# Performance work log

Measured on AMD Instinct MI355X. Metric: run time of the kernel, lower is better.

Reference implementation:

```python
import jax, jax.numpy as jnp
import numpy as np

B, T, T_OUT, D = 32, 2048, 512, 256
LN_EPS = 1e-5


def _ragged_adaptive_avg_pool(mu_mel, mel_lengths, target_lens):
    """Vectorized per-sample adaptive_avg_pool1d over ragged lengths.

    For sample b with input length L=mel_lengths[b] and output length
    O=target_lens[b], output bin j averages input frames
    [floor(j*L/O), ceil((j+1)*L/O)). Bins j >= O are zero (pad_sequence).
    Returns [B, T_OUT, D].
    """
    j = jnp.arange(T_OUT, dtype=jnp.int32)[None, :, None]   # [1, T_OUT, 1]
    t = jnp.arange(T, dtype=jnp.int32)[None, None, :]       # [1, 1, T]
    L = mel_lengths.astype(jnp.int32)[:, None, None]        # [B, 1, 1]
    O = target_lens.astype(jnp.int32)[:, None, None]        # [B, 1, 1]
    start = (j * L) // O                                     # [B, T_OUT, 1]
    end = ((j + 1) * L + O - 1) // O                         # ceil division
    valid = j < O
    w = ((t >= start) & (t < end) & valid).astype(mu_mel.dtype)  # [B, T_OUT, T]
    cnt = jnp.maximum(end - start, 1).astype(mu_mel.dtype)
    w = w / cnt
    return jnp.einsum('bjt,btd->bjd', w, mu_mel)             # [B, T_OUT, D]


def setup_inputs() -> dict:
    key = jax.random.key(0)
    k1, k2, k3, k4 = jax.random.split(key, 4)
    mu_mel = jax.random.normal(k1, (B, T, D), dtype=jnp.float32)
    mel_lengths = jax.random.randint(k2, (B,), T // 2, T + 1, dtype=jnp.int32)
    target_lens = jax.random.randint(k3, (B,), T_OUT // 2, T_OUT + 1, dtype=jnp.int32)
    conv_w = jax.random.normal(k4, (D, D), dtype=jnp.float32) * (1.0 / np.sqrt(D))
    gamma = jnp.ones((D,), dtype=jnp.float32)
    beta = jnp.zeros((D,), dtype=jnp.float32)
    return {"mu_mel": mu_mel, "mel_lengths": mel_lengths,
            "target_lens": target_lens, "conv_w": conv_w,
            "gamma": gamma, "beta": beta}


def reference(mu_mel, mel_lengths, target_lens, conv_w, gamma, beta):
    # ragged adaptive avg pool + pad into [B, T_OUT, D]; torch wraps this in
    # no_grad, so stop_gradient mirrors that.
    pooled = jax.lax.stop_gradient(
        _ragged_adaptive_avg_pool(mu_mel, mel_lengths, target_lens))
    # 1x1 Conv1d (no bias) == per-position matmul, then exact GELU
    h = jax.nn.gelu(jnp.einsum('bjd,ed->bje', pooled, conv_w), approximate=False)
    # LayerNorm over D (applied to padded positions too, as in torch)
    mean = jnp.mean(h, axis=-1, keepdims=True)
    var = jnp.mean(jnp.square(h - mean), axis=-1, keepdims=True)
    return (h - mean) * jax.lax.rsqrt(var + LN_EPS) * gamma + beta
```

## Files before the change

kernel.cpp:

```cpp
#include <hip/hip_runtime.h>

#define NB 32
#define NT 2048
#define TOUT 512
#define ND 256
#define TILE_M 16
#define BLK_J 64
#define LDA 264
#define LDH 264

typedef __attribute__((ext_vector_type(4))) float f32x4;
typedef __attribute__((ext_vector_type(8))) short bf16x8;
typedef __attribute__((ext_vector_type(4))) unsigned short u16x4;

__device__ __forceinline__ unsigned short f2b(float f) {
    unsigned int u = __builtin_bit_cast(unsigned int, f);
    return (unsigned short)((u + 0x7FFFu + ((u >> 16) & 1u)) >> 16);
}

__device__ __forceinline__ float gelu_exact(float x) {
    return 0.5f * x * (1.0f + erff(x * 0.70710678118654752440f));
}

template <int K>
__device__ __forceinline__ f32x4 sumK(const float* p) {
    f32x4 v[K];
    #pragma unroll
    for (int t = 0; t < K; ++t)
        v[t] = *reinterpret_cast<const f32x4*>(p + (size_t)t * ND);
    f32x4 s = v[0];
    #pragma unroll
    for (int t = 1; t < K; ++t) s += v[t];
    return s;
}

__global__ __launch_bounds__(256, 6)
void pool_kernel(const float* __restrict__ mu,
                 const int* __restrict__ lens,
                 const int* __restrict__ olens,
                 const float* __restrict__ wf,
                 unsigned short* __restrict__ wbF,
                 unsigned short* __restrict__ pooled)
{
    const int tid  = (int)threadIdx.x;
    const int lane = tid & 63;
    const int wv   = tid >> 6;

    if (blockIdx.y == TOUT / 4) {
        const int gid = blockIdx.x * 256 + tid;
        const int l   = gid & 63;
        const int kk  = (gid >> 6) & 7;
        const int et  = gid >> 9;
        const int e   = et * 16 + (l & 15);
        const int k   = kk * 32 + (l >> 4) * 8;
        f32x4 a = *reinterpret_cast<const f32x4*>(wf + e * ND + k);
        f32x4 c = *reinterpret_cast<const f32x4*>(wf + e * ND + k + 4);
        u16x4 p0, p1;
        p0.x = f2b(a.x); p0.y = f2b(a.y); p0.z = f2b(a.z); p0.w = f2b(a.w);
        p1.x = f2b(c.x); p1.y = f2b(c.y); p1.z = f2b(c.z); p1.w = f2b(c.w);
        *reinterpret_cast<u16x4*>(wbF + (size_t)gid * 8)     = p0;
        *reinterpret_cast<u16x4*>(wbF + (size_t)gid * 8 + 4) = p1;
        return;
    }

    const int b = blockIdx.x;
    const int j = blockIdx.y * 4 + wv;
    const int L = lens[b];
    const int O = olens[b];

    f32x4 s = {0.f, 0.f, 0.f, 0.f};
    if (j < O) {
        const int st  = (j * L) / O;
        const int en  = ((j + 1) * L + O - 1) / O;
        const int cnt = en - st;
        const float* p = mu + (size_t)(b * NT + st) * ND + lane * 4;
        switch (cnt) {
            case 2: s = sumK<2>(p); break;
            case 3: s = sumK<3>(p); break;
            case 4: s = sumK<4>(p); break;
            case 5: s = sumK<5>(p); break;
            case 6: s = sumK<6>(p); break;
            case 7: s = sumK<7>(p); break;
            case 8: s = sumK<8>(p); break;
            case 9: s = sumK<9>(p); break;
            default:
                for (int t = 0; t < cnt; ++t)
                    s += *reinterpret_cast<const f32x4*>(p + (size_t)t * ND);
                break;
        }
        s *= 1.0f / (float)cnt;
    }
    u16x4 q;
    q.x = f2b(s.x); q.y = f2b(s.y); q.z = f2b(s.z); q.w = f2b(s.w);
    *reinterpret_cast<u16x4*>(pooled + ((size_t)b * TOUT + j) * ND + lane * 4) = q;
}

__global__ __launch_bounds__(512, 2)
void mm_kernel(const unsigned short* __restrict__ pooled,
               const unsigned short* __restrict__ wbF,
               const float* __restrict__ gamma,
               const float* __restrict__ beta,
               float* __restrict__ out)
{
    __shared__ unsigned short a_lds[TILE_M * LDA];
    __shared__ float h_lds[TILE_M * LDH];

    const int b    = blockIdx.x;
    const int jb   = blockIdx.y * BLK_J;
    const int tid  = (int)threadIdx.x;
    const int lane = tid & 63;
    const int wv   = tid >> 6;
    const int r    = lane & 15;
    const int kg   = lane >> 4;

    bf16x8 wreg[8][2];
    #pragma unroll
    for (int kk = 0; kk < 8; ++kk)
        #pragma unroll
        for (int p = 0; p < 2; ++p) {
            const int et = wv * 2 + p;
            wreg[kk][p] = *reinterpret_cast<const bf16x8*>(
                wbF + (size_t)((et * 8 + kk) * 64 + lane) * 8);
        }

    const f32x4 g4 = *reinterpret_cast<const f32x4*>(&gamma[lane * 4]);
    const f32x4 b4 = *reinterpret_cast<const f32x4*>(&beta[lane * 4]);

    for (int jt = 0; jt < BLK_J / TILE_M; ++jt) {
        const int j0 = jb + jt * TILE_M;

        const unsigned short* prow = pooled + ((size_t)b * TOUT + j0) * ND;
        #pragma unroll
        for (int it = 0; it < 2; ++it) {
            const int u  = it * 512 + tid;
            const int m  = u >> 6;
            const int dd = (u & 63) * 4;
            *reinterpret_cast<u16x4*>(&a_lds[m * LDA + dd]) =
                *reinterpret_cast<const u16x4*>(prow + (size_t)u * 4);
        }
        __syncthreads();

        f32x4 acc[2];
        acc[0] = (f32x4){0.f, 0.f, 0.f, 0.f};
        acc[1] = (f32x4){0.f, 0.f, 0.f, 0.f};
        #pragma unroll
        for (int kk = 0; kk < 8; ++kk) {
            const int k0 = kk * 32 + kg * 8;
            bf16x8 af = *reinterpret_cast<const bf16x8*>(&a_lds[r * LDA + k0]);
            acc[0] = __builtin_amdgcn_mfma_f32_16x16x32_bf16(af, wreg[kk][0], acc[0], 0, 0, 0);
            acc[1] = __builtin_amdgcn_mfma_f32_16x16x32_bf16(af, wreg[kk][1], acc[1], 0, 0, 0);
        }

        #pragma unroll
        for (int p = 0; p < 2; ++p) {
            const int col = wv * 32 + p * 16 + r;
            #pragma unroll
            for (int q = 0; q < 4; ++q)
                h_lds[(kg * 4 + q) * LDH + col] = gelu_exact(acc[p][q]);
        }
        __syncthreads();

        #pragma unroll
        for (int i = 0; i < 2; ++i) {
            const int m = wv + i * 8;
            f32x4 v = *reinterpret_cast<const f32x4*>(&h_lds[m * LDH + lane * 4]);
            float s  = v.x + v.y + v.z + v.w;
            float sq = v.x * v.x + v.y * v.y + v.z * v.z + v.w * v.w;
            #pragma unroll
            for (int off = 32; off > 0; off >>= 1) {
                s  += __shfl_xor(s, off, 64);
                sq += __shfl_xor(sq, off, 64);
            }
            const float mean = s * (1.0f / 256.0f);
            const float var  = sq * (1.0f / 256.0f) - mean * mean;
            const float rs   = rsqrtf(var + 1e-5f);
            f32x4 o = (v - mean) * rs * g4 + b4;
            *reinterpret_cast<f32x4*>(&out[((size_t)(b * TOUT) + j0 + m) * ND + lane * 4]) = o;
        }
        __syncthreads();
    }
}

__global__ __launch_bounds__(256, 4)
void fused_fallback(const float* __restrict__ mu,
                    const int* __restrict__ lens,
                    const int* __restrict__ olens,
                    const float* __restrict__ wf,
                    const float* __restrict__ gamma,
                    const float* __restrict__ beta,
                    float* __restrict__ out)
{
    __shared__ unsigned short a_lds[TILE_M * LDA];
    __shared__ float h_lds[TILE_M * LDH];

    const int b    = blockIdx.x;
    const int j0   = blockIdx.y * TILE_M;
    const int tid  = (int)threadIdx.x;
    const int lane = tid & 63;
    const int wv   = tid >> 6;
    const int L = lens[b];
    const int O = olens[b];

    for (int m = wv; m < TILE_M; m += 4) {
        const int j = j0 + m;
        f32x4 acc = {0.f, 0.f, 0.f, 0.f};
        if (j < O) {
            const int s = (j * L) / O;
            const int e = ((j + 1) * L + O - 1) / O;
            const float* src = mu + (size_t)(b * NT + s) * ND + lane * 4;
            for (int t = s; t < e; ++t) {
                acc += *reinterpret_cast<const f32x4*>(src);
                src += ND;
            }
            acc *= (1.0f / (float)(e - s));
        }
        u16x4 p;
        p.x = f2b(acc.x); p.y = f2b(acc.y); p.z = f2b(acc.z); p.w = f2b(acc.w);
        *reinterpret_cast<u16x4*>(&a_lds[m * LDA + lane * 4]) = p;
    }
    __syncthreads();

    const int r  = lane & 15;
    const int kg = lane >> 4;
    const int e0 = wv * 64;
    f32x4 acc[4];
    #pragma unroll
    for (int c = 0; c < 4; ++c) acc[c] = (f32x4){0.f, 0.f, 0.f, 0.f};
    #pragma unroll
    for (int kk = 0; kk < 8; ++kk) {
        const int k0 = kk * 32 + kg * 8;
        bf16x8 af = *reinterpret_cast<const bf16x8*>(&a_lds[r * LDA + k0]);
        #pragma unroll
        for (int ct = 0; ct < 4; ++ct) {
            const int e = e0 + ct * 16 + r;
            f32x4 w0 = *reinterpret_cast<const f32x4*>(&wf[e * ND + k0]);
            f32x4 w1 = *reinterpret_cast<const f32x4*>(&wf[e * ND + k0 + 4]);
            union { bf16x8 v; unsigned short u[8]; } cv;
            cv.u[0] = f2b(w0.x); cv.u[1] = f2b(w0.y);
            cv.u[2] = f2b(w0.z); cv.u[3] = f2b(w0.w);
            cv.u[4] = f2b(w1.x); cv.u[5] = f2b(w1.y);
            cv.u[6] = f2b(w1.z); cv.u[7] = f2b(w1.w);
            acc[ct] = __builtin_amdgcn_mfma_f32_16x16x32_bf16(af, cv.v, acc[ct], 0, 0, 0);
        }
    }
    #pragma unroll
    for (int ct = 0; ct < 4; ++ct) {
        const int col  = e0 + ct * 16 + r;
        const int row0 = kg * 4;
        #pragma unroll
        for (int q = 0; q < 4; ++q)
            h_lds[(row0 + q) * LDH + col] = gelu_exact(acc[ct][q]);
    }
    __syncthreads();
    const f32x4 g4 = *reinterpret_cast<const f32x4*>(&gamma[lane * 4]);
    const f32x4 b4 = *reinterpret_cast<const f32x4*>(&beta[lane * 4]);
    #pragma unroll
    for (int i = 0; i < 4; ++i) {
        const int m = wv + i * 4;
        f32x4 v = *reinterpret_cast<const f32x4*>(&h_lds[m * LDH + lane * 4]);
        float s  = v.x + v.y + v.z + v.w;
        float sq = v.x * v.x + v.y * v.y + v.z * v.z + v.w * v.w;
        #pragma unroll
        for (int off = 32; off > 0; off >>= 1) {
            s  += __shfl_xor(s, off, 64);
            sq += __shfl_xor(sq, off, 64);
        }
        const float mean = s * (1.0f / 256.0f);
        const float var  = sq * (1.0f / 256.0f) - mean * mean;
        const float rs   = rsqrtf(var + 1e-5f);
        f32x4 o = (v - mean) * rs * g4 + b4;
        *reinterpret_cast<f32x4*>(&out[((size_t)(b * TOUT) + j0 + m) * ND + lane * 4]) = o;
    }
}

extern "C" void kernel_launch(void* const* d_in, const int* in_sizes, int n_in,
                              void* d_out, int out_size, void* d_ws, size_t ws_size,
                              hipStream_t stream) {
    const float* mu    = (const float*)d_in[0];
    const int*   lens  = (const int*)d_in[1];
    const int*   olens = (const int*)d_in[2];
    const float* wf    = (const float*)d_in[3];
    const float* gamma = (const float*)d_in[4];
    const float* beta  = (const float*)d_in[5];
    float* out = (float*)d_out;

    const size_t wb_elems = (size_t)ND * ND;
    const size_t pooled_elems = (size_t)NB * TOUT * ND;
    const size_t need = (wb_elems + pooled_elems) * sizeof(unsigned short);

    if (ws_size >= need) {
        unsigned short* wbF    = (unsigned short*)d_ws;
        unsigned short* pooled = wbF + wb_elems;
        pool_kernel<<<dim3(NB, TOUT / 4 + 1), dim3(256), 0, stream>>>(
            mu, lens, olens, wf, wbF, pooled);
        mm_kernel<<<dim3(NB, TOUT / BLK_J), dim3(512), 0, stream>>>(
            pooled, wbF, gamma, beta, out);
    } else {
        fused_fallback<<<dim3(NB, TOUT / TILE_M), dim3(256), 0, stream>>>(
            mu, lens, olens, wf, gamma, beta, out);
    }
}
```

Baseline: 28.95 us.

## Fuse ragged pooling into matmul kernel, split weight conversion into tiny kernel

After: 26.31 us. 9.1% less time.

```diff
diff --git a/kernel.cpp b/kernel.cpp
--- a/kernel.cpp
+++ b/kernel.cpp
@@ -5,7 +5,6 @@
 #define TOUT 512
 #define ND 256
 #define TILE_M 16
-#define BLK_J 64
 #define LDA 264
 #define LDH 264
 
@@ -34,79 +33,37 @@
     return s;
 }
 
-__global__ __launch_bounds__(256, 6)
-void pool_kernel(const float* __restrict__ mu,
-                 const int* __restrict__ lens,
-                 const int* __restrict__ olens,
-                 const float* __restrict__ wf,
-                 unsigned short* __restrict__ wbF,
-                 unsigned short* __restrict__ pooled)
-{
-    const int tid  = (int)threadIdx.x;
-    const int lane = tid & 63;
-    const int wv   = tid >> 6;
-
-    if (blockIdx.y == TOUT / 4) {
-        const int gid = blockIdx.x * 256 + tid;
-        const int l   = gid & 63;
-        const int kk  = (gid >> 6) & 7;
-        const int et  = gid >> 9;
-        const int e   = et * 16 + (l & 15);
-        const int k   = kk * 32 + (l >> 4) * 8;
-        f32x4 a = *reinterpret_cast<const f32x4*>(wf + e * ND + k);
-        f32x4 c = *reinterpret_cast<const f32x4*>(wf + e * ND + k + 4);
-        u16x4 p0, p1;
-        p0.x = f2b(a.x); p0.y = f2b(a.y); p0.z = f2b(a.z); p0.w = f2b(a.w);
-        p1.x = f2b(c.x); p1.y = f2b(c.y); p1.z = f2b(c.z); p1.w = f2b(c.w);
-        *reinterpret_cast<u16x4*>(wbF + (size_t)gid * 8)     = p0;
-        *reinterpret_cast<u16x4*>(wbF + (size_t)gid * 8 + 4) = p1;
-        return;
-    }
-
-    const int b = blockIdx.x;
-    const int j = blockIdx.y * 4 + wv;
-    const int L = lens[b];
-    const int O = olens[b];
-
-    f32x4 s = {0.f, 0.f, 0.f, 0.f};
-    if (j < O) {
-        const int st  = (j * L) / O;
-        const int en  = ((j + 1) * L + O - 1) / O;
-        const int cnt = en - st;
-        const float* p = mu + (size_t)(b * NT + st) * ND + lane * 4;
-        switch (cnt) {
-            case 2: s = sumK<2>(p); break;
-            case 3: s = sumK<3>(p); break;
-            case 4: s = sumK<4>(p); break;
-            case 5: s = sumK<5>(p); break;
-            case 6: s = sumK<6>(p); break;
-            case 7: s = sumK<7>(p); break;
-            case 8: s = sumK<8>(p); break;
-            case 9: s = sumK<9>(p); break;
-            default:
-                for (int t = 0; t < cnt; ++t)
-                    s += *reinterpret_cast<const f32x4*>(p + (size_t)t * ND);
-                break;
-        }
-        s *= 1.0f / (float)cnt;
-    }
-    u16x4 q;
-    q.x = f2b(s.x); q.y = f2b(s.y); q.z = f2b(s.z); q.w = f2b(s.w);
-    *reinterpret_cast<u16x4*>(pooled + ((size_t)b * TOUT + j) * ND + lane * 4) = q;
+__global__ __launch_bounds__(512)
+void cvt_w_kernel(const float* __restrict__ wf, unsigned short* __restrict__ wbF) {
+    const int gid = blockIdx.x * 512 + (int)threadIdx.x;
+    const int l   = gid & 63;
+    const int kk  = (gid >> 6) & 7;
+    const int et  = gid >> 9;
+    const int e   = et * 16 + (l & 15);
+    const int k   = kk * 32 + (l >> 4) * 8;
+    f32x4 a = *reinterpret_cast<const f32x4*>(wf + e * ND + k);
+    f32x4 c = *reinterpret_cast<const f32x4*>(wf + e * ND + k + 4);
+    u16x4 p0, p1;
+    p0.x = f2b(a.x); p0.y = f2b(a.y); p0.z = f2b(a.z); p0.w = f2b(a.w);
+    p1.x = f2b(c.x); p1.y = f2b(c.y); p1.z = f2b(c.z); p1.w = f2b(c.w);
+    *reinterpret_cast<u16x4*>(wbF + (size_t)gid * 8)     = p0;
+    *reinterpret_cast<u16x4*>(wbF + (size_t)gid * 8 + 4) = p1;
 }
 
 __global__ __launch_bounds__(512, 2)
-void mm_kernel(const unsigned short* __restrict__ pooled,
-               const unsigned short* __restrict__ wbF,
-               const float* __restrict__ gamma,
-               const float* __restrict__ beta,
-               float* __restrict__ out)
+void fused_kernel(const float* __restrict__ mu,
+                  const int* __restrict__ lens,
+                  const int* __restrict__ olens,
+                  const unsigned short* __restrict__ wbF,
+                  const float* __restrict__ gamma,
+                  const float* __restrict__ beta,
+                  float* __restrict__ out)
 {
     __shared__ unsigned short a_lds[TILE_M * LDA];
     __shared__ float h_lds[TILE_M * LDH];
 
     const int b    = blockIdx.x;
-    const int jb   = blockIdx.y * BLK_J;
+    const int j0   = blockIdx.y * TILE_M;
     const int tid  = (int)threadIdx.x;
     const int lane = tid & 63;
     const int wv   = tid >> 6;
@@ -123,61 +80,79 @@
                 wbF + (size_t)((et * 8 + kk) * 64 + lane) * 8);
         }
 
+    const int L = lens[b];
+    const int O = olens[b];
+
+    #pragma unroll
+    for (int i = 0; i < 2; ++i) {
+        const int m = wv + i * 8;
+        const int j = j0 + m;
+        f32x4 s = {0.f, 0.f, 0.f, 0.f};
+        if (j < O) {
+            const int st  = (j * L) / O;
+            const int en  = ((j + 1) * L + O - 1) / O;
+            const int cnt = en - st;
+            const float* p = mu + (size_t)(b * NT + st) * ND + lane * 4;
+            switch (cnt) {
+                case 2: s = sumK<2>(p); break;
+                case 3: s = sumK<3>(p); break;
+                case 4: s = sumK<4>(p); break;
+                case 5: s = sumK<5>(p); break;
+                case 6: s = sumK<6>(p); break;
+                case 7: s = sumK<7>(p); break;
+                case 8: s = sumK<8>(p); break;
+                case 9: s = sumK<9>(p); break;
+                default:
+                    for (int t = 0; t < cnt; ++t)
+                        s += *reinterpret_cast<const f32x4*>(p + (size_t)t * ND);
+                    break;
+            }
+            s *= 1.0f / (float)cnt;
+        }
+        u16x4 q;
+        q.x = f2b(s.x); q.y = f2b(s.y); q.z = f2b(s.z); q.w = f2b(s.w);
+        *reinterpret_cast<u16x4*>(&a_lds[m * LDA + lane * 4]) = q;
+    }
+    __syncthreads();
+
+    f32x4 acc[2];
+    acc[0] = (f32x4){0.f, 0.f, 0.f, 0.f};
+    acc[1] = (f32x4){0.f, 0.f, 0.f, 0.f};
+    #pragma unroll
+    for (int kk = 0; kk < 8; ++kk) {
+        const int k0 = kk * 32 + kg * 8;
+        bf16x8 af = *reinterpret_cast<const bf16x8*>(&a_lds[r * LDA + k0]);
+        acc[0] = __builtin_amdgcn_mfma_f32_16x16x32_bf16(af, wreg[kk][0], acc[0], 0, 0, 0);
+        acc[1] = __builtin_amdgcn_mfma_f32_16x16x32_bf16(af, wreg[kk][1], acc[1], 0, 0, 0);
+    }
+
+    #pragma unroll
+    for (int p = 0; p < 2; ++p) {
+        const int col = wv * 32 + p * 16 + r;
+        #pragma unroll
+        for (int q = 0; q < 4; ++q)
+            h_lds[(kg * 4 + q) * LDH + col] = gelu_exact(acc[p][q]);
+    }
+    __syncthreads();
+
     const f32x4 g4 = *reinterpret_cast<const f32x4*>(&gamma[lane * 4]);
     const f32x4 b4 = *reinterpret_cast<const f32x4*>(&beta[lane * 4]);
-
-    for (int jt = 0; jt < BLK_J / TILE_M; ++jt) {
-        const int j0 = jb + jt * TILE_M;
-
-        const unsigned short* prow = pooled + ((size_t)b * TOUT + j0) * ND;
-        #pragma unroll
-        for (int it = 0; it < 2; ++it) {
-            const int u  = it * 512 + tid;
-            const int m  = u >> 6;
-            const int dd = (u & 63) * 4;
-            *reinterpret_cast<u16x4*>(&a_lds[m * LDA + dd]) =
-                *reinterpret_cast<const u16x4*>(prow + (size_t)u * 4);
-        }
-        __syncthreads();
-
-        f32x4 acc[2];
-        acc[0] = (f32x4){0.f, 0.f, 0.f, 0.f};
-        acc[1] = (f32x4){0.f, 0.f, 0.f, 0.f};
-        #pragma unroll
-        for (int kk = 0; kk < 8; ++kk) {
-            const int k0 = kk * 32 + kg * 8;
-            bf16x8 af = *reinterpret_cast<const bf16x8*>(&a_lds[r * LDA + k0]);
-            acc[0] = __builtin_amdgcn_mfma_f32_16x16x32_bf16(af, wreg[kk][0], acc[0], 0, 0, 0);
-            acc[1] = __builtin_amdgcn_mfma_f32_16x16x32_bf16(af, wreg[kk][1], acc[1], 0, 0, 0);
-        }
-
-        #pragma unroll
-        for (int p = 0; p < 2; ++p) {
-            const int col = wv * 32 + p * 16 + r;
-            #pragma unroll
-            for (int q = 0; q < 4; ++q)
-                h_lds[(kg * 4 + q) * LDH + col] = gelu_exact(acc[p][q]);
-        }
-        __syncthreads();
-
-        #pragma unroll
-        for (int i = 0; i < 2; ++i) {
-            const int m = wv + i * 8;
-            f32x4 v = *reinterpret_cast<const f32x4*>(&h_lds[m * LDH + lane * 4]);
-            float s  = v.x + v.y + v.z + v.w;
-            float sq = v.x * v.x + v.y * v.y + v.z * v.z + v.w * v.w;
-            #pragma unroll
-            for (int off = 32; off > 0; off >>= 1) {
-                s  += __shfl_xor(s, off, 64);
-                sq += __shfl_xor(sq, off, 64);
-            }
-            const float mean = s * (1.0f / 256.0f);
-            const float var  = sq * (1.0f / 256.0f) - mean * mean;
-            const float rs   = rsqrtf(var + 1e-5f);
-            f32x4 o = (v - mean) * rs * g4 + b4;
-            *reinterpret_cast<f32x4*>(&out[((size_t)(b * TOUT) + j0 + m) * ND + lane * 4]) = o;
-        }
-        __syncthreads();
+    #pragma unroll
+    for (int i = 0; i < 2; ++i) {
+        const int m = wv + i * 8;
+        f32x4 v = *reinterpret_cast<const f32x4*>(&h_lds[m * LDH + lane * 4]);
+        float s  = v.x + v.y + v.z + v.w;
+        float sq = v.x * v.x + v.y * v.y + v.z * v.z + v.w * v.w;
+        #pragma unroll
+        for (int off = 32; off > 0; off >>= 1) {
+            s  += __shfl_xor(s, off, 64);
+            sq += __shfl_xor(sq, off, 64);
+        }
+        const float mean = s * (1.0f / 256.0f);
+        const float var  = sq * (1.0f / 256.0f) - mean * mean;
+        const float rs   = rsqrtf(var + 1e-5f);
+        f32x4 o = (v - mean) * rs * g4 + b4;
+        *reinterpret_cast<f32x4*>(&out[((size_t)(b * TOUT) + j0 + m) * ND + lane * 4]) = o;
     }
 }
 
@@ -284,17 +259,13 @@
     const float* beta  = (const float*)d_in[5];
     float* out = (float*)d_out;
 
-    const size_t wb_elems = (size_t)ND * ND;
-    const size_t pooled_elems = (size_t)NB * TOUT * ND;
-    const size_t need = (wb_elems + pooled_elems) * sizeof(unsigned short);
+    const size_t need = (size_t)ND * ND * sizeof(unsigned short);
 
     if (ws_size >= need) {
-        unsigned short* wbF    = (unsigned short*)d_ws;
-        unsigned short* pooled = wbF + wb_elems;
-        pool_kernel<<<dim3(NB, TOUT / 4 + 1), dim3(256), 0, stream>>>(
-            mu, lens, olens, wf, wbF, pooled);
-        mm_kernel<<<dim3(NB, TOUT / BLK_J), dim3(512), 0, stream>>>(
-            pooled, wbF, gamma, beta, out);
+        unsigned short* wbF = (unsigned short*)d_ws;
+        cvt_w_kernel<<<dim3(16), dim3(512), 0, stream>>>(wf, wbF);
+        fused_kernel<<<dim3(NB, TOUT / TILE_M), dim3(512), 0, stream>>>(
+            mu, lens, olens, wbF, gamma, beta, out);
     } else {
         fused_fallback<<<dim3(NB, TOUT / TILE_M), dim3(256), 0, stream>>>(
             mu, lens, olens, wf, gamma, beta, out);
```
